# Performance work log

Measured on AMD Instinct MI355X. Metric: run time of the kernel, lower is better.

Reference implementation:

```python
import jax, jax.numpy as jnp
import numpy as np

B, T, C = 4, 2048, 1024
N_HEAD = 16
HEAD_DIM = C // N_HEAD
SCALE = 1.0 / np.sqrt(HEAD_DIM).astype(np.float32)


def setup_inputs() -> dict:
    key = jax.random.key(0)
    ks = jax.random.split(key, 5)
    std = 1.0 / np.sqrt(C).astype(np.float32)
    return {
        "x": jax.random.normal(ks[0], (B, T, C), dtype=jnp.float32),
        "Wq": jax.random.normal(ks[1], (C, C), dtype=jnp.float32) * std,
        "Wk": jax.random.normal(ks[2], (C, C), dtype=jnp.float32) * std,
        "Wv": jax.random.normal(ks[3], (C, C), dtype=jnp.float32) * std,
        "Wo": jax.random.normal(ks[4], (C, C), dtype=jnp.float32) * std,
    }


def reference(x, Wq, Wk, Wv, Wo):
    # nn.Linear(x) == x @ W.T; projections then split heads: (B, H, T, D)
    def split_heads(t):
        return t.reshape(B, T, N_HEAD, HEAD_DIM).transpose(0, 2, 1, 3)

    q = split_heads(x @ Wq.T)
    k = split_heads(x @ Wk.T)
    v = split_heads(x @ Wv.T)

    att = jnp.einsum("bhqd,bhkd->bhqk", q, k) * SCALE  # (B, H, T, T)
    causal = jnp.tril(jnp.ones((T, T), dtype=bool))
    att = jnp.where(causal[None, None], att, -jnp.inf)
    att = jax.nn.softmax(att, axis=-1)
    # dropout = 0.0 (eval): identity
    y = jnp.einsum("bhqk,bhkd->bhqd", att, v)  # (B, H, T, D)
    y = y.transpose(0, 2, 1, 3).reshape(B, T, C)
    return y @ Wo.T
```

## Files before the change

kernel.cpp:

```cpp
#include <hip/hip_runtime.h>
#include <stdint.h>

#define B_SZ   4
#define T_SEQ  2048
#define C_DIM  1024
#define N_HEAD 16
#define HEAD_D 64
#define QSCALE 0.18033688011112042f

typedef unsigned short u16;
typedef unsigned int   u32;
typedef __bf16  bfv8  __attribute__((ext_vector_type(8)));
typedef float   f32x4 __attribute__((ext_vector_type(4)));

__device__ __forceinline__ u16 f2bf_hu(float f) {
  union { float f; u32 i; } u; u.f = f;
  return (u16)((u.i + 0x8000u) >> 16);
}
__device__ __forceinline__ u32 pkbf16(float a, float b) {
  union { float f; u32 i; } ua, ub; ua.f = a; ub.f = b;
  return __builtin_amdgcn_perm(ub.i + 0x8000u, ua.i + 0x8000u, 0x07060302u);
}
__device__ __forceinline__ float fexp2(float x) {
#if __has_builtin(__builtin_amdgcn_exp2f)
  return __builtin_amdgcn_exp2f(x);
#else
  return __expf(x * 0.69314718f);
#endif
}

__device__ __forceinline__ void async_cp16(const u16* __restrict__ g, u16* l) {
  __builtin_amdgcn_global_load_lds(
      (const __attribute__((address_space(1))) void*)g,
      (__attribute__((address_space(3))) void*)l, 16, 0, 0);
}

__global__ __launch_bounds__(256) void cvt_all_kernel(
    const float* __restrict__ x,  const float* __restrict__ W0,
    const float* __restrict__ W1, const float* __restrict__ W2,
    const float* __restrict__ W3, u16* __restrict__ dst) {
  int bid = blockIdx.x;
  const float* s; u16* d; int local;
  if (bid < 8192) {
    s = x; d = dst; local = bid;
  } else {
    int w = (bid - 8192) >> 10;
    local  = (bid - 8192) & 1023;
    s = (w == 0) ? W0 : (w == 1) ? W1 : (w == 2) ? W2 : W3;
    d = dst + (size_t)(B_SZ * T_SEQ * C_DIM) + (size_t)w * (C_DIM * C_DIM);
  }
  int i = local * 256 + threadIdx.x;
  float4 v = ((const float4*)s)[i];
  int2 o; o.x = (int)pkbf16(v.x, v.y); o.y = (int)pkbf16(v.z, v.w);
  ((int2*)d)[i] = o;
}

__device__ __forceinline__ void mfma_step(const u16* Sbuf, int wm, int wn,
                                          int frow, int fk, f32x4 acc[4][4]) {
  const u16* As = Sbuf;
  const u16* Bs = Sbuf + 4096;
  bfv8 af[4], bfr[4];
#pragma unroll
  for (int mt = 0; mt < 4; mt++)
    af[mt] = *(const bfv8*)(As + (wm * 64 + mt * 16 + frow) * 32 + fk);
#pragma unroll
  for (int nt = 0; nt < 4; nt++)
    bfr[nt] = *(const bfv8*)(Bs + (wn * 64 + nt * 16 + frow) * 32 + fk);
  __builtin_amdgcn_s_setprio(1);
#pragma unroll
  for (int mt = 0; mt < 4; mt++)
#pragma unroll
    for (int nt = 0; nt < 4; nt++)
      acc[mt][nt] = __builtin_amdgcn_mfma_f32_16x16x32_bf16(
          af[mt], bfr[nt], acc[mt][nt], 0, 0, 0);
  __builtin_amdgcn_s_setprio(0);
}

__device__ __forceinline__ void gemm_core(const u16* __restrict__ A,
                                          const u16* __restrict__ Bw,
                                          int m0, int n0,
                                          f32x4 acc[4][4],
                                          u16* smem) {
  const int tid  = threadIdx.x;
  const int wave = tid >> 6;
  const int lane = tid & 63;
  const int frow = lane & 15;
  const int fk   = (lane >> 4) * 8;
  const int wm   = wave >> 1, wn = wave & 1;

  const int lrow = tid >> 2;
  const int lcol = (tid & 3) * 8;
  const u16* ga0 = A  + (size_t)(m0 + lrow)      * C_DIM + lcol;
  const u16* ga1 = A  + (size_t)(m0 + 64 + lrow) * C_DIM + lcol;
  const u16* gb0 = Bw + (size_t)(n0 + lrow)      * C_DIM + lcol;
  const u16* gb1 = Bw + (size_t)(n0 + 64 + lrow) * C_DIM + lcol;
  u16* b0 = smem;
  u16* b1 = smem + 8192;
  u16* b2 = smem + 16384;
  const int so = tid * 8;

#define STAGE_TO(dst) do {                        \
    async_cp16(ga0, (dst) + so);                  \
    async_cp16(ga1, (dst) + 2048 + so);           \
    async_cp16(gb0, (dst) + 4096 + so);           \
    async_cp16(gb1, (dst) + 6144 + so);           \
    ga0 += 32; ga1 += 32; gb0 += 32; gb1 += 32;   \
  } while (0)
#define WAIT4_BAR do {                                      \
    asm volatile("s_waitcnt vmcnt(4)" ::: "memory");        \
    __builtin_amdgcn_s_barrier();                           \
  } while (0)

  STAGE_TO(b0);
  STAGE_TO(b1);
  WAIT4_BAR;

#pragma unroll 1
  for (int ii = 0; ii < 30; ii += 3) {
    STAGE_TO(b2);
    mfma_step(b0, wm, wn, frow, fk, acc);
    WAIT4_BAR;

    STAGE_TO(b0);
    mfma_step(b1, wm, wn, frow, fk, acc);
    WAIT4_BAR;

    STAGE_TO(b1);
    mfma_step(b2, wm, wn, frow, fk, acc);
    WAIT4_BAR;
  }
  mfma_step(b0, wm, wn, frow, fk, acc);
  asm volatile("s_waitcnt vmcnt(0)" ::: "memory");
  __builtin_amdgcn_s_barrier();
  mfma_step(b1, wm, wn, frow, fk, acc);
#undef STAGE_TO
#undef WAIT4_BAR
}

__global__ __launch_bounds__(256) void gemm_qkv_kernel(
    const u16* __restrict__ X, const u16* __restrict__ Wq,
    const u16* __restrict__ Wk, const u16* __restrict__ Wv,
    u16* __restrict__ Qo, u16* __restrict__ Ko, u16* __restrict__ Vo) {
  __shared__ __align__(16) u16 smem[24576];
  const u16* W = (blockIdx.z == 0) ? Wq : (blockIdx.z == 1) ? Wk : Wv;
  u16* dst     = (blockIdx.z == 0) ? Qo : (blockIdx.z == 1) ? Ko : Vo;
  const int m0 = blockIdx.x * 128, n0 = blockIdx.y * 128;

  f32x4 acc[4][4];
#pragma unroll
  for (int i = 0; i < 4; i++)
#pragma unroll
    for (int j = 0; j < 4; j++) acc[i][j] = {0.f, 0.f, 0.f, 0.f};

  gemm_core(X, W, m0, n0, acc, smem);
  __syncthreads();

  const int lane = threadIdx.x & 63, wave = threadIdx.x >> 6;
  const int wm = wave >> 1, wn = wave & 1;
  const int quad = lane >> 4, col = lane & 15;
  u16* buf = smem + wave * 4096;
  const int bb = (m0 + wm * 64) >> 11;
  const int t0 = (m0 + wm * 64) & (T_SEQ - 1);
  const int h  = (n0 >> 6) + wn;

  if (blockIdx.z == 2) {
#pragma unroll
    for (int mt = 0; mt < 4; mt++)
#pragma unroll
      for (int nt = 0; nt < 4; nt++) {
        int d_l = nt * 16 + col;
        int g   = mt * 4 + quad;
        int gp  = g ^ (d_l & 15);
        int2 o;
        o.x = (int)pkbf16(acc[mt][nt][0], acc[mt][nt][1]);
        o.y = (int)pkbf16(acc[mt][nt][2], acc[mt][nt][3]);
        *(int2*)(buf + d_l * 64 + gp * 4) = o;
      }
#pragma unroll
    for (int tt = 0; tt < 8; tt++) {
      int d_l = tt * 8 + (lane >> 3);
      int seg = lane & 7;
      int g0 = (2 * seg) ^ (d_l & 15), g1 = (2 * seg + 1) ^ (d_l & 15);
      int2 a  = *(const int2*)(buf + d_l * 64 + g0 * 4);
      int2 bv = *(const int2*)(buf + d_l * 64 + g1 * 4);
      int4 o; o.x = a.x; o.y = a.y; o.z = bv.x; o.w = bv.y;
      *(int4*)(Vo + (((size_t)(bb * N_HEAD + h) * HEAD_D + d_l) * T_SEQ
                     + t0 + seg * 8)) = o;
    }
  } else {
    const float sc = (blockIdx.z == 0) ? QSCALE : 1.0f;
#pragma unroll
    for (int mt = 0; mt < 4; mt++)
#pragma unroll
      for (int nt = 0; nt < 4; nt++)
#pragma unroll
        for (int r = 0; r < 4; r++) {
          int m_l = mt * 16 + quad * 4 + r;
          int n_l = nt * 16 + col;
          int gp = (n_l >> 3) ^ (m_l & 7);
          buf[m_l * 64 + gp * 8 + (n_l & 7)] = f2bf_hu(acc[mt][nt][r] * sc);
        }
#pragma unroll
    for (int tt = 0; tt < 8; tt++) {
      int m_l = tt * 8 + (lane >> 3);
      int seg = lane & 7;
      int gp = seg ^ (m_l & 7);
      int4 o = *(const int4*)(buf + m_l * 64 + gp * 8);
      *(int4*)(dst + (((size_t)(bb * N_HEAD + h) * T_SEQ + t0 + m_l) * HEAD_D
                      + seg * 8)) = o;
    }
  }
}

__global__ __launch_bounds__(256) void gemm_out_kernel(
    const u16* __restrict__ Y, const u16* __restrict__ Wo,
    float* __restrict__ Out) {
  __shared__ __align__(16) u16 smem[24576];
  const int m0 = blockIdx.x * 128, n0 = blockIdx.y * 128;

  f32x4 acc[4][4];
#pragma unroll
  for (int i = 0; i < 4; i++)
#pragma unroll
    for (int j = 0; j < 4; j++) acc[i][j] = {0.f, 0.f, 0.f, 0.f};

  gemm_core(Y, Wo, m0, n0, acc, smem);
  __syncthreads();

  const int lane = threadIdx.x & 63, wave = threadIdx.x >> 6;
  const int wm = wave >> 1, wn = wave & 1;
  const int quad = lane >> 4, col = lane & 15;
  float* bufF = (float*)(smem + wave * 4096);

#pragma unroll
  for (int c = 0; c < 2; c++) {
#pragma unroll
    for (int mt = 0; mt < 4; mt++)
#pragma unroll
      for (int nn = 0; nn < 2; nn++)
#pragma unroll
        for (int r = 0; r < 4; r++) {
          int nt = 2 * c + nn;
          int m_l = mt * 16 + quad * 4 + r;
          int n_l = nn * 16 + col;
          int gp = (n_l >> 2) ^ (m_l & 7);
          bufF[m_l * 32 + gp * 4 + (n_l & 3)] = acc[mt][nt][r];
        }
#pragma unroll
    for (int tt = 0; tt < 8; tt++) {
      int m_l = tt * 8 + (lane >> 3);
      int seg = lane & 7;
      int gp = seg ^ (m_l & 7);
      float4 o = *(const float4*)(bufF + m_l * 32 + gp * 4);
      *(float4*)(Out + (size_t)(m0 + wm * 64 + m_l) * C_DIM
                 + n0 + wn * 64 + c * 32 + seg * 4) = o;
    }
  }
}

#define ATT_Q 128

__global__ __launch_bounds__(256, 3) void attn_kernel(
    const u16* __restrict__ Qg, const u16* __restrict__ Kg,
    const u16* __restrict__ Vtg, u16* __restrict__ Yg) {
  __shared__ __align__(16) u16 QPs[128 * 64];
  __shared__ __align__(16) u16 Ks[2 * 64 * 64];
  __shared__ __align__(16) u16 Vt[2 * 64 * 64];

  const int tid = threadIdx.x;
  const int wave = tid >> 6, lane = tid & 63;
  const int quad = lane >> 4, l15 = lane & 15;
  const int bh = blockIdx.x;
  const int b = bh >> 4, h = bh & 15;
  const int yy = blockIdx.y, gq = yy >> 2, rq = yy & 3;
  const int qt = (gq == 0) ? 15 - rq : (gq == 1) ? rq
               : (gq == 2) ? 11 - rq : 4 + rq;
  const int q0 = qt * ATT_Q;

  const u16* Kbase = Kg  + (size_t)bh * T_SEQ * HEAD_D;
  const u16* Vbase = Vtg + (size_t)bh * HEAD_D * T_SEQ;
  const int trow = tid >> 3;
  const int gx   = (tid & 7) ^ (trow & 7);

#define STAGE_KV(slot, kt_) do {                                          \
    const u16* ks0 = Kbase + (size_t)(((kt_) << 6) + trow) * HEAD_D + gx * 8; \
    const u16* vs0 = Vbase + (size_t)trow * T_SEQ + ((kt_) << 6) + gx * 8;    \
    u16* kd = Ks + (slot) * 4096 + tid * 8;                               \
    u16* vd = Vt + (slot) * 4096 + tid * 8;                               \
    async_cp16(ks0, kd);                                                  \
    async_cp16(ks0 + 32 * HEAD_D, kd + 2048);                             \
    async_cp16(vs0, vd);                                                  \
    async_cp16(vs0 + (size_t)32 * T_SEQ, vd + 2048);                      \
  } while (0)

  STAGE_KV(0, 0);

  {
    const int row = tid >> 1;
    const int c0 = (tid & 1) * 32;
    const u16* gp = Qg + ((size_t)bh * T_SEQ + q0 + row) * HEAD_D + c0;
#pragma unroll
    for (int g = 0; g < 4; g++) {
      int4 v = *(const int4*)(gp + g * 8);
      int pg = ((c0 >> 3) + g) ^ (row & 7);
      *(int4*)(QPs + row * 64 + pg * 8) = v;
    }
  }
  __syncthreads();

  bfv8 qb[2][2];
#pragma unroll
  for (int nt = 0; nt < 2; nt++)
#pragma unroll
    for (int ks = 0; ks < 2; ks++) {
      int q = wave * 32 + nt * 16 + l15;
      int pg = (ks * 4 + quad) ^ (q & 7);
      qb[nt][ks] = *(const bfv8*)(QPs + q * 64 + pg * 8);
    }

  float l_i[2] = {0.f, 0.f};
  f32x4 ao[4][2];
#pragma unroll
  for (int mt = 0; mt < 4; mt++)
#pragma unroll
    for (int nt = 0; nt < 2; nt++) ao[mt][nt] = {0.f, 0.f, 0.f, 0.f};

  const int ktmax = 2 * qt + 1;
  for (int kt = 0; kt <= ktmax; kt++) {
    if (kt < ktmax) STAGE_KV((kt + 1) & 1, kt + 1);
    const u16* Ksb = Ks + (kt & 1) * 4096;
    const u16* Vtb = Vt + (kt & 1) * 4096;

    f32x4 as[4][2];
#pragma unroll
    for (int mt = 0; mt < 4; mt++)
#pragma unroll
      for (int nt = 0; nt < 2; nt++) as[mt][nt] = {0.f, 0.f, 0.f, 0.f};
#pragma unroll
    for (int mt = 0; mt < 4; mt++) {
      bfv8 ka[2];
#pragma unroll
      for (int ks = 0; ks < 2; ks++) {
        int key = mt * 16 + l15;
        int pg = (ks * 4 + quad) ^ (key & 7);
        ka[ks] = *(const bfv8*)(Ksb + key * 64 + pg * 8);
      }
#pragma unroll
      for (int nt = 0; nt < 2; nt++)
#pragma unroll
        for (int ks = 0; ks < 2; ks++)
          as[mt][nt] = __builtin_amdgcn_mfma_f32_16x16x32_bf16(
              ka[ks], qb[nt][ks], as[mt][nt], 0, 0, 0);
    }

    const bool diag = (kt >= 2 * qt);
#pragma unroll
    for (int nt = 0; nt < 2; nt++) {
      const int q_l = wave * 32 + nt * 16 + l15;
      const int q_g = q0 + q_l;
      float lacc = 0.f;
#pragma unroll
      for (int mt = 0; mt < 4; mt++) {
        float p[4];
#pragma unroll
        for (int r = 0; r < 4; r++) {
          float s = as[mt][nt][r];
          if (diag) {
            int key_g = kt * 64 + mt * 16 + quad * 4 + r;
            if (key_g > q_g) s = -1e30f;
          }
          p[r] = fexp2(s);
        }
        lacc += (p[0] + p[1]) + (p[2] + p[3]);
        int pg = (2 * mt + (quad >> 1)) ^ (q_l & 7);
        int2 o;
        o.x = (int)pkbf16(p[0], p[1]);
        o.y = (int)pkbf16(p[2], p[3]);
        *(int2*)(QPs + q_l * 64 + pg * 8 + (quad & 1) * 4) = o;
      }
      l_i[nt] += lacc;
    }

    bfv8 pf[2][2];
#pragma unroll
    for (int nt = 0; nt < 2; nt++)
#pragma unroll
      for (int ks = 0; ks < 2; ks++) {
        int q_l = wave * 32 + nt * 16 + l15;
        int pg = (ks * 4 + quad) ^ (q_l & 7);
        pf[nt][ks] = *(const bfv8*)(QPs + q_l * 64 + pg * 8);
      }
#pragma unroll
    for (int mt = 0; mt < 4; mt++) {
      bfv8 va[2];
#pragma unroll
      for (int ks = 0; ks < 2; ks++) {
        int d = mt * 16 + l15;
        int pg = (ks * 4 + quad) ^ (d & 7);
        va[ks] = *(const bfv8*)(Vtb + d * 64 + pg * 8);
      }
#pragma unroll
      for (int nt = 0; nt < 2; nt++)
#pragma unroll
        for (int ks = 0; ks < 2; ks++)
          ao[mt][nt] = __builtin_amdgcn_mfma_f32_16x16x32_bf16(
              va[ks], pf[nt][ks], ao[mt][nt], 0, 0, 0);
    }

    asm volatile("s_waitcnt vmcnt(0)" ::: "memory");
    __builtin_amdgcn_s_barrier();
  }
#undef STAGE_KV

#pragma unroll
  for (int nt = 0; nt < 2; nt++) {
    l_i[nt] += __shfl_xor(l_i[nt], 16);
    l_i[nt] += __shfl_xor(l_i[nt], 32);
  }

  __syncthreads();
#pragma unroll
  for (int nt = 0; nt < 2; nt++) {
    float inv = 1.0f / l_i[nt];
    int q_l = wave * 32 + nt * 16 + l15;
#pragma unroll
    for (int mt = 0; mt < 4; mt++) {
      int g = mt * 4 + quad;
      int gp = g ^ (q_l & 15);
      int2 o;
      o.x = (int)pkbf16(ao[mt][nt][0] * inv, ao[mt][nt][1] * inv);
      o.y = (int)pkbf16(ao[mt][nt][2] * inv, ao[mt][nt][3] * inv);
      *(int2*)(QPs + q_l * 64 + gp * 4) = o;
    }
  }
  __syncthreads();
#pragma unroll
  for (int rr = 0; rr < 4; rr++) {
    int q   = rr * 32 + (tid >> 3);
    int seg = tid & 7;
    int g0 = (2 * seg) ^ (q & 15), g1 = (2 * seg + 1) ^ (q & 15);
    int2 a  = *(const int2*)(QPs + q * 64 + g0 * 4);
    int2 bv = *(const int2*)(QPs + q * 64 + g1 * 4);
    int4 o; o.x = a.x; o.y = a.y; o.z = bv.x; o.w = bv.y;
    *(int4*)(Yg + ((size_t)b * T_SEQ + q0 + q) * C_DIM + h * HEAD_D + seg * 8) = o;
  }
}

extern "C" void kernel_launch(void* const* d_in, const int* in_sizes, int n_in,
                              void* d_out, int out_size, void* d_ws, size_t ws_size,
                              hipStream_t stream) {
  const float* x  = (const float*)d_in[0];
  const float* Wq = (const float*)d_in[1];
  const float* Wk = (const float*)d_in[2];
  const float* Wv = (const float*)d_in[3];
  const float* Wo = (const float*)d_in[4];
  float* out = (float*)d_out;

  const size_t NE = (size_t)B_SZ * T_SEQ * C_DIM;
  const size_t NW = (size_t)C_DIM * C_DIM;
  u16* xbf = (u16*)d_ws;
  u16* wqb = xbf + NE;
  u16* wkb = wqb + NW;
  u16* wvb = wkb + NW;
  u16* wob = wvb + NW;
  u16* qws = wob + NW;
  u16* kws = qws + NE;
  u16* vws = kws + NE;
  u16* yws = vws + NE;

  cvt_all_kernel<<<8192 + 4096, 256, 0, stream>>>(x, Wq, Wk, Wv, Wo, xbf);

  dim3 g1(T_SEQ * B_SZ / 128, C_DIM / 128, 3);
  gemm_qkv_kernel<<<g1, 256, 0, stream>>>(xbf, wqb, wkb, wvb, qws, kws, vws);

  dim3 g2(B_SZ * N_HEAD, T_SEQ / ATT_Q);
  attn_kernel<<<g2, 256, 0, stream>>>(qws, kws, vws, yws);

  dim3 g3(T_SEQ * B_SZ / 128, C_DIM / 128);
  gemm_out_kernel<<<g3, 256, 0, stream>>>(yws, wob, out);
}
```

Measured before the change: 236.3 us.

## Load GEMM B operand directly into registers, stage only A through LDS

The shared GEMM core no longer stages the weight (B) tile through shared memory. Each wave now loads its B fragments straight from global memory into registers, double-buffered one k-step ahead, and only the A tile goes through the triple-buffered async LDS pipeline. This halves LDS traffic and footprint per step, shrinking smem from 24576 to 16384 elements, which may allow higher occupancy. The trade-off is that B reads are no longer shared between the two waves in the same column. Global loads become uncoalesced 16-byte row fetches, and the extra registers holding B may cost occupancy or add latency exposure.

```diff
diff --git a/kernel.cpp b/kernel.cpp
--- a/kernel.cpp
+++ b/kernel.cpp
@@ -55,24 +55,21 @@
   ((int2*)d)[i] = o;
 }
 
-__device__ __forceinline__ void mfma_step(const u16* Sbuf, int wm, int wn,
-                                          int frow, int fk, f32x4 acc[4][4]) {
-  const u16* As = Sbuf;
-  const u16* Bs = Sbuf + 4096;
-  bfv8 af[4], bfr[4];
+__device__ __forceinline__ void mfma_stepB(const u16* As, int wm, int frow,
+                                           int fk, bfv8 b0, bfv8 b1, bfv8 b2,
+                                           bfv8 b3, f32x4 acc[4][4]) {
+  bfv8 af[4];
 #pragma unroll
   for (int mt = 0; mt < 4; mt++)
     af[mt] = *(const bfv8*)(As + (wm * 64 + mt * 16 + frow) * 32 + fk);
-#pragma unroll
-  for (int nt = 0; nt < 4; nt++)
-    bfr[nt] = *(const bfv8*)(Bs + (wn * 64 + nt * 16 + frow) * 32 + fk);
   __builtin_amdgcn_s_setprio(1);
 #pragma unroll
-  for (int mt = 0; mt < 4; mt++)
-#pragma unroll
-    for (int nt = 0; nt < 4; nt++)
-      acc[mt][nt] = __builtin_amdgcn_mfma_f32_16x16x32_bf16(
-          af[mt], bfr[nt], acc[mt][nt], 0, 0, 0);
+  for (int mt = 0; mt < 4; mt++) {
+    acc[mt][0] = __builtin_amdgcn_mfma_f32_16x16x32_bf16(af[mt], b0, acc[mt][0], 0, 0, 0);
+    acc[mt][1] = __builtin_amdgcn_mfma_f32_16x16x32_bf16(af[mt], b1, acc[mt][1], 0, 0, 0);
+    acc[mt][2] = __builtin_amdgcn_mfma_f32_16x16x32_bf16(af[mt], b2, acc[mt][2], 0, 0, 0);
+    acc[mt][3] = __builtin_amdgcn_mfma_f32_16x16x32_bf16(af[mt], b3, acc[mt][3], 0, 0, 0);
+  }
   __builtin_amdgcn_s_setprio(0);
 }
 
@@ -90,58 +87,65 @@
 
   const int lrow = tid >> 2;
   const int lcol = (tid & 3) * 8;
-  const u16* ga0 = A  + (size_t)(m0 + lrow)      * C_DIM + lcol;
-  const u16* ga1 = A  + (size_t)(m0 + 64 + lrow) * C_DIM + lcol;
-  const u16* gb0 = Bw + (size_t)(n0 + lrow)      * C_DIM + lcol;
-  const u16* gb1 = Bw + (size_t)(n0 + 64 + lrow) * C_DIM + lcol;
+  const u16* ga0 = A + (size_t)(m0 + lrow)      * C_DIM + lcol;
+  const u16* ga1 = A + (size_t)(m0 + 64 + lrow) * C_DIM + lcol;
+  const u16* gB  = Bw + (size_t)(n0 + wn * 64 + frow) * C_DIM + fk;
   u16* b0 = smem;
-  u16* b1 = smem + 8192;
-  u16* b2 = smem + 16384;
+  u16* b1 = smem + 4096;
+  u16* b2 = smem + 8192;
   const int so = tid * 8;
-
-#define STAGE_TO(dst) do {                        \
+  bfv8 Be0, Be1, Be2, Be3, Bo0, Bo1, Bo2, Bo3;
+
+#define STAGE_A(dst) do {                         \
     async_cp16(ga0, (dst) + so);                  \
     async_cp16(ga1, (dst) + 2048 + so);           \
-    async_cp16(gb0, (dst) + 4096 + so);           \
-    async_cp16(gb1, (dst) + 6144 + so);           \
-    ga0 += 32; ga1 += 32; gb0 += 32; gb1 += 32;   \
+    ga0 += 32; ga1 += 32;                         \
   } while (0)
-#define WAIT4_BAR do {                                      \
-    asm volatile("s_waitcnt vmcnt(4)" ::: "memory");        \
-    __builtin_amdgcn_s_barrier();                           \
+#define LOAD_B(b) do {                            \
+    b##0 = *(const bfv8*)(gB);                    \
+    b##1 = *(const bfv8*)(gB + 16 * C_DIM);       \
+    b##2 = *(const bfv8*)(gB + 32 * C_DIM);       \
+    b##3 = *(const bfv8*)(gB + 48 * C_DIM);       \
+    gB += 32;                                     \
   } while (0)
-
-  STAGE_TO(b0);
-  STAGE_TO(b1);
-  WAIT4_BAR;
+#define GSTEP(bufc, bufn2, B0_, B1_, B2_, B3_, BN) do {   \
+    LOAD_B(BN);                                           \
+    STAGE_A(bufn2);                                       \
+    mfma_stepB(bufc, wm, frow, fk, B0_, B1_, B2_, B3_, acc); \
+    asm volatile("s_waitcnt vmcnt(2)" ::: "memory");      \
+    __builtin_amdgcn_s_barrier();                         \
+  } while (0)
+
+  STAGE_A(b0);
+  LOAD_B(Be);
+  STAGE_A(b1);
+  asm volatile("s_waitcnt vmcnt(2)" ::: "memory");
+  __builtin_amdgcn_s_barrier();
 
 #pragma unroll 1
-  for (int ii = 0; ii < 30; ii += 3) {
-    STAGE_TO(b2);
-    mfma_step(b0, wm, wn, frow, fk, acc);
-    WAIT4_BAR;
-
-    STAGE_TO(b0);
-    mfma_step(b1, wm, wn, frow, fk, acc);
-    WAIT4_BAR;
-
-    STAGE_TO(b1);
-    mfma_step(b2, wm, wn, frow, fk, acc);
-    WAIT4_BAR;
-  }
-  mfma_step(b0, wm, wn, frow, fk, acc);
+  for (int ii = 0; ii < 5; ii++) {
+    GSTEP(b0, b2, Be0, Be1, Be2, Be3, Bo);
+    GSTEP(b1, b0, Bo0, Bo1, Bo2, Bo3, Be);
+    GSTEP(b2, b1, Be0, Be1, Be2, Be3, Bo);
+    GSTEP(b0, b2, Bo0, Bo1, Bo2, Bo3, Be);
+    GSTEP(b1, b0, Be0, Be1, Be2, Be3, Bo);
+    GSTEP(b2, b1, Bo0, Bo1, Bo2, Bo3, Be);
+  }
+  LOAD_B(Bo);
+  mfma_stepB(b0, wm, frow, fk, Be0, Be1, Be2, Be3, acc);
   asm volatile("s_waitcnt vmcnt(0)" ::: "memory");
   __builtin_amdgcn_s_barrier();
-  mfma_step(b1, wm, wn, frow, fk, acc);
-#undef STAGE_TO
-#undef WAIT4_BAR
+  mfma_stepB(b1, wm, frow, fk, Bo0, Bo1, Bo2, Bo3, acc);
+#undef STAGE_A
+#undef LOAD_B
+#undef GSTEP
 }
 
 __global__ __launch_bounds__(256) void gemm_qkv_kernel(
     const u16* __restrict__ X, const u16* __restrict__ Wq,
     const u16* __restrict__ Wk, const u16* __restrict__ Wv,
     u16* __restrict__ Qo, u16* __restrict__ Ko, u16* __restrict__ Vo) {
-  __shared__ __align__(16) u16 smem[24576];
+  __shared__ __align__(16) u16 smem[16384];
   const u16* W = (blockIdx.z == 0) ? Wq : (blockIdx.z == 1) ? Wk : Wv;
   u16* dst     = (blockIdx.z == 0) ? Qo : (blockIdx.z == 1) ? Ko : Vo;
   const int m0 = blockIdx.x * 128, n0 = blockIdx.y * 128;
@@ -215,7 +219,7 @@
 __global__ __launch_bounds__(256) void gemm_out_kernel(
     const u16* __restrict__ Y, const u16* __restrict__ Wo,
     float* __restrict__ Out) {
-  __shared__ __align__(16) u16 smem[24576];
+  __shared__ __align__(16) u16 smem[16384];
   const int m0 = blockIdx.x * 128, n0 = blockIdx.y * 128;
 
   f32x4 acc[4][4];
```

After: 296.1 us. 1.25x slower.
